# Kernel tuning notes

Measured on AMD Instinct MI355X. Metric: run time of the kernel, lower is better.

## Reference

```python
import jax, jax.numpy as jnp
import numpy as np

TEMPERATURE = 0.07
IGNORE_LABEL = -1
EPS = 1e-8


def setup_inputs() -> dict:
    key = jax.random.key(0)
    k1, k2, k3 = jax.random.split(key, 3)
    N = 100000
    E = 6400000
    edge_index = jax.random.randint(k1, (2, E), 0, N, dtype=jnp.int64)
    edge_logits = jax.random.normal(k2, (E,), dtype=jnp.float32)
    label = jax.random.randint(k3, (N,), 0, 20, dtype=jnp.int64)
    return {"edge_index": edge_index, "edge_logits": edge_logits, "label": label}


def reference(edge_index, edge_logits, label):
    N = label.shape[0]
    idx_i = edge_index[0]
    idx_j = edge_index[1]
    label_i = label[idx_i]
    label_j = label[idx_j]
    valid = (label_i != IGNORE_LABEL) & (label_j != IGNORE_LABEL)
    is_pos = (label_i == label_j) & valid
    is_neg = (label_i != label_j) & valid

    # node is a boundary node if it has at least one valid negative edge
    neg_count = jax.ops.segment_sum(is_neg.astype(jnp.float32), idx_i, num_segments=N)
    is_boundary = (neg_count > 0) & (label != IGNORE_LABEL)

    # edges whose source node is a boundary node (torch filters invalid edges first)
    edge_is_boundary = is_boundary[idx_i] & valid
    exp_logits = jnp.exp(edge_logits / TEMPERATURE)
    w = jnp.where(edge_is_boundary, exp_logits, 0.0)

    denominator = jax.ops.segment_sum(w, idx_i, num_segments=N)
    numerator = jax.ops.segment_sum(jnp.where(is_pos, w, 0.0), idx_i, num_segments=N)

    valid_boundary = is_boundary & (denominator > 0)
    per_node = jnp.where(
        valid_boundary,
        jnp.log(denominator + EPS) - jnp.log(numerator + EPS),
        0.0,
    )
    count = jnp.maximum(jnp.sum(valid_boundary.astype(jnp.float32)), 1.0)
    return jnp.sum(per_node) / count
```

## Files before the change

kernel.cpp:

```cpp
#include <hip/hip_runtime.h>

#define INV_T  (1.0f / 0.07f)
#define EPS    1e-8f

#define RSH     11
#define RNODES  (1 << RSH)
#define GSPLIT  16
#define SBLK    256
#define EPT     8
#define EPB     (SBLK * EPT)
#define MAXB    256

__global__ void cbl_pack_lab8(const int* __restrict__ label,
                              unsigned char* __restrict__ lab8, int N) {
    int i = blockIdx.x * blockDim.x + threadIdx.x;
    if (i < N) {
        int v = label[i];
        lab8[i] = (v == -1) ? 0xFFu : (unsigned char)v;
    }
}

__global__ __launch_bounds__(SBLK) void cbl_scatter(
    const int* __restrict__ idx_i,
    const int* __restrict__ idx_j,
    const float* __restrict__ logits,
    const unsigned char* __restrict__ lab8,
    unsigned* __restrict__ table,
    uint2* __restrict__ payload,
    int E, int B) {
    __shared__ unsigned s_cnt[4][MAXB];
    __shared__ unsigned s_wb[4][MAXB];
    __shared__ unsigned s_tot[MAXB];
    __shared__ unsigned s_pref[MAXB];
    __shared__ uint2    s_stage[EPB];

    const int wave = threadIdx.x >> 6;
    const int lane = threadIdx.x & 63;

    for (int t = threadIdx.x; t < B; t += SBLK) {
        s_cnt[0][t] = 0; s_cnt[1][t] = 0; s_cnt[2][t] = 0; s_cnt[3][t] = 0;
    }
    __syncthreads();

    const int blockStart = blockIdx.x * EPB;
    int           iarr[EPT];
    float         warr[EPT];
    unsigned char ljarr[EPT];

#pragma unroll
    for (int q = 0; q < EPT / 4; ++q) {
        int base = blockStart + (q * SBLK + threadIdx.x) * 4;
        if (base < E) {
            int4   ii = *reinterpret_cast<const int4*>(idx_i + base);
            int4   jj = *reinterpret_cast<const int4*>(idx_j + base);
            float4 lg = *reinterpret_cast<const float4*>(logits + base);
            iarr[q * 4 + 0] = ii.x; iarr[q * 4 + 1] = ii.y;
            iarr[q * 4 + 2] = ii.z; iarr[q * 4 + 3] = ii.w;
            ljarr[q * 4 + 0] = lab8[jj.x]; ljarr[q * 4 + 1] = lab8[jj.y];
            ljarr[q * 4 + 2] = lab8[jj.z]; ljarr[q * 4 + 3] = lab8[jj.w];
            warr[q * 4 + 0] = __expf(lg.x * INV_T);
            warr[q * 4 + 1] = __expf(lg.y * INV_T);
            warr[q * 4 + 2] = __expf(lg.z * INV_T);
            warr[q * 4 + 3] = __expf(lg.w * INV_T);
            atomicAdd(&s_cnt[wave][(ii.x >> RSH) & (MAXB - 1)], 1u);
            atomicAdd(&s_cnt[wave][(ii.y >> RSH) & (MAXB - 1)], 1u);
            atomicAdd(&s_cnt[wave][(ii.z >> RSH) & (MAXB - 1)], 1u);
            atomicAdd(&s_cnt[wave][(ii.w >> RSH) & (MAXB - 1)], 1u);
        } else {
            iarr[q * 4 + 0] = iarr[q * 4 + 1] = -1;
            iarr[q * 4 + 2] = iarr[q * 4 + 3] = -1;
            warr[q * 4 + 0] = warr[q * 4 + 1] = 0.0f;
            warr[q * 4 + 2] = warr[q * 4 + 3] = 0.0f;
            ljarr[q * 4 + 0] = ljarr[q * 4 + 1] = 0xFFu;
            ljarr[q * 4 + 2] = ljarr[q * 4 + 3] = 0xFFu;
        }
    }
    __syncthreads();

    for (int t = threadIdx.x; t < B; t += SBLK)
        s_tot[t] = s_cnt[0][t] + s_cnt[1][t] + s_cnt[2][t] + s_cnt[3][t];
    __syncthreads();

    if (B <= 64) {
        if (threadIdx.x < 64) {
            unsigned v = (lane < B) ? s_tot[lane] : 0u;
            unsigned incl = v;
            for (int off = 1; off < 64; off <<= 1) {
                unsigned n = __shfl_up(incl, off, 64);
                if (lane >= off) incl += n;
            }
            if (lane < B) s_pref[lane] = incl - v;
        }
    } else {
        if (threadIdx.x == 0) {
            unsigned r = 0;
            for (int b = 0; b < B; ++b) { s_pref[b] = r; r += s_tot[b]; }
        }
    }
    __syncthreads();

    for (int t = threadIdx.x; t < B; t += SBLK) {
        unsigned pref = s_pref[t];
        table[(size_t)blockIdx.x * B + t] = (pref << 16) | s_tot[t];
        unsigned gb = pref;
        s_wb[0][t] = gb;  gb += s_cnt[0][t];
        s_wb[1][t] = gb;  gb += s_cnt[1][t];
        s_wb[2][t] = gb;  gb += s_cnt[2][t];
        s_wb[3][t] = gb;
        s_cnt[0][t] = 0; s_cnt[1][t] = 0; s_cnt[2][t] = 0; s_cnt[3][t] = 0;
    }
    __syncthreads();

#pragma unroll
    for (int k = 0; k < EPT; ++k) {
        int i = iarr[k];
        if (i < 0) continue;
        int b = (i >> RSH) & (MAXB - 1);
        unsigned slot = s_wb[wave][b] + atomicAdd(&s_cnt[wave][b], 1u);
        unsigned meta = (unsigned)(i & (RNODES - 1)) | ((unsigned)ljarr[k] << RSH);
        s_stage[slot] = make_uint2(meta, __float_as_uint(warr[k]));
    }
    __syncthreads();

    int lim = E - blockStart; if (lim > EPB) lim = EPB;
    int lim4 = lim >> 1;
    const uint4* src4 = reinterpret_cast<const uint4*>(s_stage);
    uint4* dst4 = reinterpret_cast<uint4*>(payload + blockStart);
    for (int t = threadIdx.x; t < lim4; t += SBLK) dst4[t] = src4[t];
}

__global__ __launch_bounds__(256) void cbl_accum(
    const uint2* __restrict__ payload,
    const unsigned* __restrict__ table,
    const unsigned char* __restrict__ lab8,
    float* __restrict__ partials,
    int N, int B, int nBlk) {
    int b = blockIdx.x / GSPLIT;
    int g = blockIdx.x % GSPLIT;

    __shared__ float         acc[RNODES * 2];
    __shared__ unsigned char slab[RNODES];

    for (int t = threadIdx.x; t < RNODES * 2; t += 256) acc[t] = 0.0f;
    int nodeBase = b << RSH;
    for (int t = threadIdx.x; t < RNODES; t += 256) {
        int n = nodeBase + t;
        slab[t] = (n < N) ? lab8[n] : 0xFFu;
    }
    __syncthreads();

    int wave = threadIdx.x >> 6, lane = threadIdx.x & 63;
    for (int c = g * 4 + wave; c < nBlk; c += GSPLIT * 4) {
        unsigned tbl  = table[(size_t)c * B + b];
        unsigned cnt  = tbl & 0xFFFFu;
        unsigned start = (unsigned)c * EPB + (tbl >> 16);
        for (unsigned k = lane; k < cnt; k += 64) {
            uint2 p = payload[start + k];
            unsigned local = p.x & (RNODES - 1);
            unsigned lj    = (p.x >> RSH) & 0xFFu;
            unsigned li    = slab[local];
            if (li == 0xFFu || lj == 0xFFu) continue;
            atomicAdd(&acc[(local << 1) | (li == lj ? 1 : 0)],
                      __uint_as_float(p.y));
        }
    }
    __syncthreads();

    float* dst = partials + (size_t)blockIdx.x * (RNODES * 2);
    for (int t = threadIdx.x; t < RNODES * 2; t += 256) dst[t] = acc[t];
}

__global__ __launch_bounds__(256) void cbl_loss(
    const float* __restrict__ partials,
    float* __restrict__ acc2, int N) {
    float lsum = 0.0f, lcnt = 0.0f;
    int stride = gridDim.x * blockDim.x;
    for (int n = blockIdx.x * blockDim.x + threadIdx.x; n < N; n += stride) {
        int b = n >> RSH;
        int local = n & (RNODES - 1);
        float neg = 0.0f, pos = 0.0f;
#pragma unroll 4
        for (int g = 0; g < GSPLIT; ++g) {
            const float* p = partials
                + (size_t)(b * GSPLIT + g) * (RNODES * 2) + local * 2;
            float2 v = *reinterpret_cast<const float2*>(p);
            neg += v.x;
            pos += v.y;
        }
        if (neg > 0.0f) {
            lsum += logf(neg + pos + EPS) - logf(pos + EPS);
            lcnt += 1.0f;
        }
    }
    for (int off = 32; off > 0; off >>= 1) {
        lsum += __shfl_down(lsum, off, 64);
        lcnt += __shfl_down(lcnt, off, 64);
    }
    __shared__ float s_sum[4];
    __shared__ float s_cnt2[4];
    int wid = threadIdx.x >> 6, lane = threadIdx.x & 63;
    if (lane == 0) { s_sum[wid] = lsum; s_cnt2[wid] = lcnt; }
    __syncthreads();
    if (threadIdx.x == 0) {
        float bs = 0.0f, bc = 0.0f;
        for (int w = 0; w < 4; ++w) { bs += s_sum[w]; bc += s_cnt2[w]; }
        atomicAdd(&acc2[0], bs);
        atomicAdd(&acc2[1], bc);
    }
}

__global__ void cbl_finalize(const float* __restrict__ acc2,
                             float* __restrict__ out) {
    out[0] = acc2[0] / fmaxf(acc2[1], 1.0f);
}

__global__ __launch_bounds__(256) void cbl_edge_fb(
    const int* __restrict__ idx_i, const int* __restrict__ idx_j,
    const float* __restrict__ logits, const unsigned char* __restrict__ lab8,
    float* __restrict__ buf, int E) {
    int stride = gridDim.x * blockDim.x;
    for (int e = blockIdx.x * blockDim.x + threadIdx.x; e < E; e += stride) {
        unsigned char li = lab8[idx_i[e]];
        unsigned char lj = lab8[idx_j[e]];
        if (li == 0xFFu || lj == 0xFFu) continue;
        float w = __expf(logits[e] * INV_T);
        int slot = (idx_i[e] << 1) | (li == lj ? 1 : 0);
        atomicAdd(&buf[slot], w);
    }
}

__global__ __launch_bounds__(256) void cbl_loss_fb(
    const float* __restrict__ buf, float* __restrict__ acc2, int N) {
    float lsum = 0.0f, lcnt = 0.0f;
    int stride = gridDim.x * blockDim.x;
    for (int n = blockIdx.x * blockDim.x + threadIdx.x; n < N; n += stride) {
        float neg = buf[2 * n], pos = buf[2 * n + 1];
        if (neg > 0.0f) {
            lsum += logf(neg + pos + EPS) - logf(pos + EPS);
            lcnt += 1.0f;
        }
    }
    for (int off = 32; off > 0; off >>= 1) {
        lsum += __shfl_down(lsum, off, 64);
        lcnt += __shfl_down(lcnt, off, 64);
    }
    __shared__ float s_sum[4];
    __shared__ float s_cnt2[4];
    int wid = threadIdx.x >> 6, lane = threadIdx.x & 63;
    if (lane == 0) { s_sum[wid] = lsum; s_cnt2[wid] = lcnt; }
    __syncthreads();
    if (threadIdx.x == 0) {
        float bs = 0.0f, bc = 0.0f;
        for (int w = 0; w < 4; ++w) { bs += s_sum[w]; bc += s_cnt2[w]; }
        atomicAdd(&acc2[0], bs);
        atomicAdd(&acc2[1], bc);
    }
}

extern "C" void kernel_launch(void* const* d_in, const int* in_sizes, int n_in,
                              void* d_out, int out_size, void* d_ws, size_t ws_size,
                              hipStream_t stream) {
    const int*   edge_index = (const int*)d_in[0];
    const float* logits     = (const float*)d_in[1];
    const int*   label      = (const int*)d_in[2];

    const int E = in_sizes[1];
    const int N = in_sizes[2];
    const int* idx_i = edge_index;
    const int* idx_j = edge_index + E;

    const int B    = (N + RNODES - 1) >> RSH;
    const int nBlk = (E + EPB - 1) / EPB;
    const int block = 256;

    char* p = (char*)d_ws;
    float*    acc2   = (float*)p;               p += 16;
    unsigned char* lab8 = (unsigned char*)p;    p += ((size_t)N + 15) & ~(size_t)15;
    unsigned* table  = (unsigned*)p;            p += (((size_t)nBlk * B * 4) + 15) & ~(size_t)15;
    uint2*    payload = (uint2*)p;              p += (size_t)E * 8;
    float*    partials = (float*)p;             p += (size_t)B * GSPLIT * RNODES * 2 * 4;
    size_t need = (size_t)(p - (char*)d_ws);

    const bool fast = (ws_size >= need) && ((E & 3) == 0) && (E >= 4) &&
                      (B >= 1) && (B <= MAXB) &&
                      (((uintptr_t)payload & 15) == 0);

    if (fast) {
        hipMemsetAsync(acc2, 0, 8, stream);
        cbl_pack_lab8<<<(N + block - 1) / block, block, 0, stream>>>(label, lab8, N);

        cbl_scatter<<<nBlk, SBLK, 0, stream>>>(idx_i, idx_j, logits, lab8,
                                               table, payload, E, B);

        cbl_accum<<<B * GSPLIT, block, 0, stream>>>(payload, table, lab8,
                                                    partials, N, B, nBlk);

        int g5 = (N + block - 1) / block; if (g5 > 1024) g5 = 1024;
        cbl_loss<<<g5, block, 0, stream>>>(partials, acc2, N);
        cbl_finalize<<<1, 1, 0, stream>>>(acc2, (float*)d_out);
    } else {
        float* buf = (float*)d_ws;
        float* facc = buf + (size_t)2 * N;
        unsigned char* flab = (unsigned char*)(facc + 2);
        hipMemsetAsync(d_ws, 0, (size_t)N * 8 + 8, stream);
        cbl_pack_lab8<<<(N + block - 1) / block, block, 0, stream>>>(label, flab, N);
        int ge = (E + block - 1) / block; if (ge > 8192) ge = 8192;
        cbl_edge_fb<<<ge, block, 0, stream>>>(idx_i, idx_j, logits, flab, buf, E);
        int g5 = (N + block - 1) / block; if (g5 > 1024) g5 = 1024;
        cbl_loss_fb<<<g5, block, 0, stream>>>(buf, facc, N);
        cbl_finalize<<<1, 1, 0, stream>>>(facc, (float*)d_out);
    }
}
```

Before: 107.1 us.

## Pack edge payload into 32 bits with fp16 scaled logit and pos flag

The scatter pass now looks up both endpoint labels and packs each edge into one 32-bit word: the half-precision scaled logit (-inf for invalid edges), a positive-pair bit and the local node index. This halves payload write and read traffic, and the accumulate kernel no longer needs the label tile or the validity check. Exponentiation moves to the accumulate pass. GSPLIT doubles to spread accumulation across more blocks, which also doubles the partials buffer the loss kernel must read. The fp16 rounding of logits around 70 gives noticeable relative error in the exp weights, which is an accuracy risk.

```diff
diff --git a/kernel.cpp b/kernel.cpp
--- a/kernel.cpp
+++ b/kernel.cpp
@@ -1,11 +1,12 @@
 #include <hip/hip_runtime.h>
+#include <hip/hip_fp16.h>
 
 #define INV_T  (1.0f / 0.07f)
 #define EPS    1e-8f
 
 #define RSH     11
 #define RNODES  (1 << RSH)
-#define GSPLIT  16
+#define GSPLIT  32
 #define SBLK    256
 #define EPT     8
 #define EPB     (SBLK * EPT)
@@ -26,13 +27,13 @@
     const float* __restrict__ logits,
     const unsigned char* __restrict__ lab8,
     unsigned* __restrict__ table,
-    uint2* __restrict__ payload,
+    unsigned* __restrict__ payload,
     int E, int B) {
     __shared__ unsigned s_cnt[4][MAXB];
     __shared__ unsigned s_wb[4][MAXB];
     __shared__ unsigned s_tot[MAXB];
     __shared__ unsigned s_pref[MAXB];
-    __shared__ uint2    s_stage[EPB];
+    __shared__ __align__(16) unsigned s_stage[EPB];
 
     const int wave = threadIdx.x >> 6;
     const int lane = threadIdx.x & 63;
@@ -43,9 +44,8 @@
     __syncthreads();
 
     const int blockStart = blockIdx.x * EPB;
-    int           iarr[EPT];
-    float         warr[EPT];
-    unsigned char ljarr[EPT];
+    int      barr[EPT];
+    unsigned marr[EPT];
 
 #pragma unroll
     for (int q = 0; q < EPT / 4; ++q) {
@@ -54,25 +54,27 @@
             int4   ii = *reinterpret_cast<const int4*>(idx_i + base);
             int4   jj = *reinterpret_cast<const int4*>(idx_j + base);
             float4 lg = *reinterpret_cast<const float4*>(logits + base);
-            iarr[q * 4 + 0] = ii.x; iarr[q * 4 + 1] = ii.y;
-            iarr[q * 4 + 2] = ii.z; iarr[q * 4 + 3] = ii.w;
-            ljarr[q * 4 + 0] = lab8[jj.x]; ljarr[q * 4 + 1] = lab8[jj.y];
-            ljarr[q * 4 + 2] = lab8[jj.z]; ljarr[q * 4 + 3] = lab8[jj.w];
-            warr[q * 4 + 0] = __expf(lg.x * INV_T);
-            warr[q * 4 + 1] = __expf(lg.y * INV_T);
-            warr[q * 4 + 2] = __expf(lg.z * INV_T);
-            warr[q * 4 + 3] = __expf(lg.w * INV_T);
-            atomicAdd(&s_cnt[wave][(ii.x >> RSH) & (MAXB - 1)], 1u);
-            atomicAdd(&s_cnt[wave][(ii.y >> RSH) & (MAXB - 1)], 1u);
-            atomicAdd(&s_cnt[wave][(ii.z >> RSH) & (MAXB - 1)], 1u);
-            atomicAdd(&s_cnt[wave][(ii.w >> RSH) & (MAXB - 1)], 1u);
+            int iv[4] = {ii.x, ii.y, ii.z, ii.w};
+            int jv[4] = {jj.x, jj.y, jj.z, jj.w};
+            float lv[4] = {lg.x, lg.y, lg.z, lg.w};
+#pragma unroll
+            for (int r = 0; r < 4; ++r) {
+                unsigned char li = lab8[iv[r]];
+                unsigned char lj = lab8[jv[r]];
+                bool valid = (li != 0xFFu) && (lj != 0xFFu);
+                unsigned hb = valid
+                    ? (unsigned)__half_as_ushort(__float2half(lv[r] * INV_T))
+                    : 0xFC00u;
+                unsigned pos = (valid && li == lj) ? 1u : 0u;
+                marr[q * 4 + r] = (hb << 16) | (pos << 11)
+                                | ((unsigned)iv[r] & (RNODES - 1));
+                int b = (iv[r] >> RSH) & (MAXB - 1);
+                barr[q * 4 + r] = b;
+                atomicAdd(&s_cnt[wave][b], 1u);
+            }
         } else {
-            iarr[q * 4 + 0] = iarr[q * 4 + 1] = -1;
-            iarr[q * 4 + 2] = iarr[q * 4 + 3] = -1;
-            warr[q * 4 + 0] = warr[q * 4 + 1] = 0.0f;
-            warr[q * 4 + 2] = warr[q * 4 + 3] = 0.0f;
-            ljarr[q * 4 + 0] = ljarr[q * 4 + 1] = 0xFFu;
-            ljarr[q * 4 + 2] = ljarr[q * 4 + 3] = 0xFFu;
+#pragma unroll
+            for (int r = 0; r < 4; ++r) barr[q * 4 + r] = -1;
         }
     }
     __syncthreads();
@@ -113,40 +115,31 @@
 
 #pragma unroll
     for (int k = 0; k < EPT; ++k) {
-        int i = iarr[k];
-        if (i < 0) continue;
-        int b = (i >> RSH) & (MAXB - 1);
+        int b = barr[k];
+        if (b < 0) continue;
         unsigned slot = s_wb[wave][b] + atomicAdd(&s_cnt[wave][b], 1u);
-        unsigned meta = (unsigned)(i & (RNODES - 1)) | ((unsigned)ljarr[k] << RSH);
-        s_stage[slot] = make_uint2(meta, __float_as_uint(warr[k]));
+        s_stage[slot] = marr[k];
     }
     __syncthreads();
 
     int lim = E - blockStart; if (lim > EPB) lim = EPB;
-    int lim4 = lim >> 1;
+    int lim4 = lim >> 2;
     const uint4* src4 = reinterpret_cast<const uint4*>(s_stage);
     uint4* dst4 = reinterpret_cast<uint4*>(payload + blockStart);
     for (int t = threadIdx.x; t < lim4; t += SBLK) dst4[t] = src4[t];
 }
 
 __global__ __launch_bounds__(256) void cbl_accum(
-    const uint2* __restrict__ payload,
+    const unsigned* __restrict__ payload,
     const unsigned* __restrict__ table,
-    const unsigned char* __restrict__ lab8,
     float* __restrict__ partials,
-    int N, int B, int nBlk) {
+    int B, int nBlk) {
     int b = blockIdx.x / GSPLIT;
     int g = blockIdx.x % GSPLIT;
 
-    __shared__ float         acc[RNODES * 2];
-    __shared__ unsigned char slab[RNODES];
+    __shared__ float acc[RNODES * 2];
 
     for (int t = threadIdx.x; t < RNODES * 2; t += 256) acc[t] = 0.0f;
-    int nodeBase = b << RSH;
-    for (int t = threadIdx.x; t < RNODES; t += 256) {
-        int n = nodeBase + t;
-        slab[t] = (n < N) ? lab8[n] : 0xFFu;
-    }
     __syncthreads();
 
     int wave = threadIdx.x >> 6, lane = threadIdx.x & 63;
@@ -155,13 +148,10 @@
         unsigned cnt  = tbl & 0xFFFFu;
         unsigned start = (unsigned)c * EPB + (tbl >> 16);
         for (unsigned k = lane; k < cnt; k += 64) {
-            uint2 p = payload[start + k];
-            unsigned local = p.x & (RNODES - 1);
-            unsigned lj    = (p.x >> RSH) & 0xFFu;
-            unsigned li    = slab[local];
-            if (li == 0xFFu || lj == 0xFFu) continue;
-            atomicAdd(&acc[(local << 1) | (li == lj ? 1 : 0)],
-                      __uint_as_float(p.y));
+            unsigned p = payload[start + k];
+            float x = __half2float(__ushort_as_half((unsigned short)(p >> 16)));
+            float w = __expf(x);
+            atomicAdd(&acc[((p & (RNODES - 1)) << 1) | ((p >> 11) & 1u)], w);
         }
     }
     __syncthreads();
@@ -277,7 +267,7 @@
     float*    acc2   = (float*)p;               p += 16;
     unsigned char* lab8 = (unsigned char*)p;    p += ((size_t)N + 15) & ~(size_t)15;
     unsigned* table  = (unsigned*)p;            p += (((size_t)nBlk * B * 4) + 15) & ~(size_t)15;
-    uint2*    payload = (uint2*)p;              p += (size_t)E * 8;
+    unsigned* payload = (unsigned*)p;           p += (((size_t)E * 4) + 15) & ~(size_t)15;
     float*    partials = (float*)p;             p += (size_t)B * GSPLIT * RNODES * 2 * 4;
     size_t need = (size_t)(p - (char*)d_ws);
 
@@ -292,8 +282,8 @@
         cbl_scatter<<<nBlk, SBLK, 0, stream>>>(idx_i, idx_j, logits, lab8,
                                                table, payload, E, B);
 
-        cbl_accum<<<B * GSPLIT, block, 0, stream>>>(payload, table, lab8,
-                                                    partials, N, B, nBlk);
+        cbl_accum<<<B * GSPLIT, block, 0, stream>>>(payload, table,
+                                                    partials, B, nBlk);
 
         int g5 = (N + block - 1) / block; if (g5 > 1024) g5 = 1024;
         cbl_loss<<<g5, block, 0, stream>>>(partials, acc2, N);
```

Measured after the change: 118.8 us. 1.11x slower.
